# Optimization experiments

Hardware: AMD Instinct MI355X
Metric: run time of the kernel (lower is better)

## Reference

```python
import jax, jax.numpy as jnp
import numpy as np


def _mlp(x, w1, b1, w2, b2):
    # generic 2-layer MLP (stand-in for ConfiguredModule's combine_mlp / embedding_mlp)
    return jax.nn.gelu(x @ w1 + b1) @ w2 + b2


def setup_inputs() -> dict:
    key = jax.random.key(0)
    ks = jax.random.split(key, 8)
    B, N, A = 8, 128, 64          # molecules, atoms, nfeature
    Rr, Ra = 32, 16               # radial / angular geometry shifts
    P = N * (N - 1) // 2          # 8128 atom pairs
    d_pair, H, nembed = 32, 512, 256

    def rnd(k, shp, scale=1.0):
        return jax.random.normal(k, shp, dtype=jnp.float32) * scale

    return {
        "gr": rnd(ks[0], (B, N, Rr, N), 0.1),
        "ga": rnd(ks[1], (B, N, Ra, P), 0.1),
        "afv": rnd(ks[2], (B, N, A)),
        # combine_mlp: 2A -> 2A -> d_pair
        "cw1": rnd(ks[3], (2 * A, 2 * A), 1.0 / np.sqrt(2 * A)),
        "cb1": jnp.zeros((2 * A,), jnp.float32),
        "cw2": rnd(ks[4], (2 * A, d_pair), 1.0 / np.sqrt(2 * A)),
        "cb2": jnp.zeros((d_pair,), jnp.float32),
        # embedding_mlp: Rr*A + Ra*d_pair -> H -> nembed
        "ew1": rnd(ks[5], (Rr * A + Ra * d_pair, H), 1.0 / np.sqrt(Rr * A + Ra * d_pair)),
        "eb1": jnp.zeros((H,), jnp.float32),
        "ew2": rnd(ks[6], (H, nembed), 1.0 / np.sqrt(H)),
        "eb2": jnp.zeros((nembed,), jnp.float32),
    }


def reference(gr, ga, afv, cw1, cb1, cw2, cb2, ew1, eb1, ew2, eb2):
    B, N, A = afv.shape
    # _combine_afv_1: pairwise outer sum/product, upper-triangular (i<j) pairs.
    # Instead of materializing [B, 2A, N, N] and masking, gather pairs directly
    # (row-major i<j order matches torch's triu boolean-mask indexing).
    ii, jj = jnp.triu_indices(N, k=1)           # [P]
    ai = afv[:, ii, :]                           # [B, P, A]
    aj = afv[:, jj, :]                           # [B, P, A]
    afv_pair = jnp.concatenate([ai + aj, ai * aj], axis=-1)  # [B, P, 2A]
    afv_pair = _mlp(afv_pair, cw1, cb1, cw2, cb2)            # [B, P, d_pair]

    # grv = matmul(gr, afv[:, None]) : [B, N, Rr, N] @ [B, 1, N, A] -> [B, N, Rr, A]
    grv = jnp.einsum('bnrm,bma->bnra', gr, afv).reshape(B, N, -1)
    # gav = matmul(ga, afv_pair[:, None]) : [B, N, Ra, P] @ [B, 1, P, d] -> [B, N, Ra, d]
    gav = jnp.einsum('bnap,bpd->bnad', ga, afv_pair).reshape(B, N, -1)

    aef = _mlp(jnp.concatenate([grv, gav], axis=-1), ew1, eb1, ew2, eb2)  # [B, N, nembed]
    return aef, afv
```

## Files before the change

### kernel.cpp

```cpp
#include <hip/hip_runtime.h>
#include <math.h>

#define BB 8
#define NN 128
#define AA 64
#define RR 32
#define RA 16
#define PP 8128
#define DP 32
#define HH 512
#define EE 256
#define XDIM 2560

static constexpr size_t WS_PAIRT = 0;
static constexpr size_t WS_XB    = WS_PAIRT + (size_t)BB*DP*PP/2;
static constexpr size_t WS_EW1B  = WS_XB + (size_t)BB*NN*XDIM/2;
static constexpr size_t WS_CW1T  = WS_EW1B + (size_t)HH*XDIM/2;
static constexpr size_t WS_CW2T  = WS_CW1T + (size_t)128*128/2;
static constexpr size_t WS_EW2B  = WS_CW2T + (size_t)DP*128/2;
static constexpr size_t WS_HB    = WS_EW2B + (size_t)EE*HH/2;

typedef __attribute__((ext_vector_type(8))) short bf16x8;
typedef __attribute__((ext_vector_type(4))) float f32x4;

__device__ __forceinline__ float gelu_f(float x) {
    float u = 0.7978845608028654f * (x + 0.044715f * x * x * x);
    float au = fabsf(u);
    float e = __expf(-2.0f * au);
    float th = (1.0f - e) / (1.0f + e);
    th = copysignf(th, u);
    return 0.5f * x * (1.0f + th);
}

__device__ __forceinline__ unsigned short f2bf(float x) {
    union { float f; unsigned u; } v; v.f = x;
    unsigned r = v.u + 0x7fffu + ((v.u >> 16) & 1u);
    return (unsigned short)(r >> 16);
}

__device__ __forceinline__ bf16x8 pack_bf16x8(float4 a, float4 b) {
    bf16x8 r;
    r[0] = (short)f2bf(a.x); r[1] = (short)f2bf(a.y);
    r[2] = (short)f2bf(a.z); r[3] = (short)f2bf(a.w);
    r[4] = (short)f2bf(b.x); r[5] = (short)f2bf(b.y);
    r[6] = (short)f2bf(b.z); r[7] = (short)f2bf(b.w);
    return r;
}

__global__ __launch_bounds__(256) void prep_k(
    const float* __restrict__ cw1, const float* __restrict__ cw2,
    unsigned short* __restrict__ cw1T, unsigned short* __restrict__ cw2T)
{
    const int bid = blockIdx.x, t = threadIdx.x;
    if (bid < 16) {
        int idx = bid * 256 + t;
        int n = idx >> 5;
        int k0 = (idx & 31) * 4;
        ushort4 o;
        o.x = f2bf(cw1[(size_t)(k0 + 0) * 128 + n]);
        o.y = f2bf(cw1[(size_t)(k0 + 1) * 128 + n]);
        o.z = f2bf(cw1[(size_t)(k0 + 2) * 128 + n]);
        o.w = f2bf(cw1[(size_t)(k0 + 3) * 128 + n]);
        *(ushort4*)(cw1T + (size_t)n * 128 + k0) = o;
    } else {
        int idx = (bid - 16) * 256 + t;
        int d = idx >> 5;
        int k0 = (idx & 31) * 4;
        ushort4 o;
        o.x = f2bf(cw2[(size_t)(k0 + 0) * DP + d]);
        o.y = f2bf(cw2[(size_t)(k0 + 1) * DP + d]);
        o.z = f2bf(cw2[(size_t)(k0 + 2) * DP + d]);
        o.w = f2bf(cw2[(size_t)(k0 + 3) * DP + d]);
        *(ushort4*)(cw2T + (size_t)d * 128 + k0) = o;
    }
}

__global__ __launch_bounds__(256) void stage1_k(
    const float* __restrict__ afv, const unsigned short* __restrict__ cw1T,
    const float* __restrict__ cb1, const unsigned short* __restrict__ cw2T,
    const float* __restrict__ cb2, unsigned short* __restrict__ pairT)
{
    __shared__ unsigned short sm[16384];
    __shared__ int iis[64], jjs[64];
    const int bid = blockIdx.x;
    const int t = threadIdx.x;
    const int w = t >> 6, lane = t & 63;
    const int lm = lane & 15, lg = lane >> 4;

    const int b = bid / 127;
    const int pbase = (bid % 127) * 64;
    unsigned short* X = sm;
    unsigned short* Hs = sm + 8192;

    if (t < 64) {
        int p = pbase + t;
        int i = 0;
        while (i < 126) {
            int nx = i + 1;
            int off = nx * 127 - (nx * (nx - 1)) / 2;
            if (off <= p) i = nx; else break;
        }
        int off = i * 127 - (i * (i - 1)) / 2;
        iis[t] = i;
        jjs[t] = i + 1 + (p - off);
    }
    __syncthreads();
    {
        int pp = t & 63, seg = t >> 6;
        const float* ar = afv + (size_t)(b * NN + iis[pp]) * AA + seg * 16;
        const float* br = afv + (size_t)(b * NN + jjs[pp]) * AA + seg * 16;
        float4 xa = *(const float4*)(ar),     xb2 = *(const float4*)(ar + 4);
        float4 xc = *(const float4*)(ar + 8), xd = *(const float4*)(ar + 12);
        float4 ya = *(const float4*)(br),     yb = *(const float4*)(br + 4);
        float4 yc = *(const float4*)(br + 8), yd = *(const float4*)(br + 12);
        float4 s0 = make_float4(xa.x + ya.x, xa.y + ya.y, xa.z + ya.z, xa.w + ya.w);
        float4 s1 = make_float4(xb2.x + yb.x, xb2.y + yb.y, xb2.z + yb.z, xb2.w + yb.w);
        float4 s2 = make_float4(xc.x + yc.x, xc.y + yc.y, xc.z + yc.z, xc.w + yc.w);
        float4 s3 = make_float4(xd.x + yd.x, xd.y + yd.y, xd.z + yd.z, xd.w + yd.w);
        float4 p0 = make_float4(xa.x * ya.x, xa.y * ya.y, xa.z * ya.z, xa.w * ya.w);
        float4 p1 = make_float4(xb2.x * yb.x, xb2.y * yb.y, xb2.z * yb.z, xb2.w * yb.w);
        float4 p2 = make_float4(xc.x * yc.x, xc.y * yc.y, xc.z * yc.z, xc.w * yc.w);
        float4 p3 = make_float4(xd.x * yd.x, xd.y * yd.y, xd.z * yd.z, xd.w * yd.w);
        int gs = seg * 2, gp = 8 + seg * 2, sw = pp & 7;
        *(bf16x8*)(X + pp * 128 + (((gs + 0) ^ sw) * 8)) = pack_bf16x8(s0, s1);
        *(bf16x8*)(X + pp * 128 + (((gs + 1) ^ sw) * 8)) = pack_bf16x8(s2, s3);
        *(bf16x8*)(X + pp * 128 + (((gp + 0) ^ sw) * 8)) = pack_bf16x8(p0, p1);
        *(bf16x8*)(X + pp * 128 + (((gp + 1) ^ sw) * 8)) = pack_bf16x8(p2, p3);
    }
    __syncthreads();
    const int wn = w * 32;
    f32x4 acc1[4][2];
    #pragma unroll
    for (int i = 0; i < 4; ++i)
        #pragma unroll
        for (int j = 0; j < 2; ++j) acc1[i][j] = 0.f;
    #pragma unroll
    for (int ks = 0; ks < 4; ++ks) {
        int g = ks * 4 + lg;
        bf16x8 a[4];
        #pragma unroll
        for (int mi = 0; mi < 4; ++mi) {
            int row = mi * 16 + lm;
            a[mi] = *(const bf16x8*)(X + row * 128 + ((g ^ (row & 7)) * 8));
        }
        #pragma unroll
        for (int ni = 0; ni < 2; ++ni) {
            bf16x8 bv = *(const bf16x8*)(cw1T + (size_t)(wn + ni * 16 + lm) * 128 +
                                         ks * 32 + lg * 8);
            #pragma unroll
            for (int mi = 0; mi < 4; ++mi)
                acc1[mi][ni] = __builtin_amdgcn_mfma_f32_16x16x32_bf16(
                    a[mi], bv, acc1[mi][ni], 0, 0, 0);
        }
    }
    #pragma unroll
    for (int ni = 0; ni < 2; ++ni) {
        int n = wn + ni * 16 + lm;
        float bb = cb1[n];
        int gn = n >> 3, ne = n & 7;
        #pragma unroll
        for (int mi = 0; mi < 4; ++mi)
            #pragma unroll
            for (int r = 0; r < 4; ++r) {
                int row = mi * 16 + lg * 4 + r;
                Hs[row * 128 + ((gn ^ (row & 7)) * 8 + ne)] =
                    f2bf(gelu_f(acc1[mi][ni][r] + bb));
            }
    }
    __syncthreads();
    f32x4 acc2[2];
    acc2[0] = 0.f; acc2[1] = 0.f;
    #pragma unroll
    for (int ks = 0; ks < 4; ++ks) {
        int row = w * 16 + lm;
        int g = ks * 4 + lg;
        bf16x8 a2 = *(const bf16x8*)(Hs + row * 128 + ((g ^ (row & 7)) * 8));
        #pragma unroll
        for (int ni = 0; ni < 2; ++ni) {
            bf16x8 bv = *(const bf16x8*)(cw2T + (size_t)(ni * 16 + lm) * 128 +
                                         ks * 32 + lg * 8);
            acc2[ni] = __builtin_amdgcn_mfma_f32_16x16x32_bf16(a2, bv, acc2[ni], 0, 0, 0);
        }
    }
    {
        unsigned short* T = sm;
        __syncthreads();
        #pragma unroll
        for (int ni = 0; ni < 2; ++ni) {
            int d = ni * 16 + lm;
            float bb = cb2[d];
            #pragma unroll
            for (int r = 0; r < 4; ++r) {
                int p = w * 16 + lg * 4 + r;
                T[d * 64 + p] = f2bf(acc2[ni][r] + bb);
            }
        }
        __syncthreads();
        int d = t >> 3, slot = t & 7;
        bf16x8 v = *(const bf16x8*)(T + d * 64 + slot * 8);
        *(bf16x8*)(pairT + ((size_t)b * DP + d) * PP + pbase + slot * 8) = v;
    }
}

__global__ __launch_bounds__(256) void gav_k(
    const float* __restrict__ ga, const unsigned short* __restrict__ pairT,
    unsigned short* __restrict__ Xb,
    const float* __restrict__ gr, const float* __restrict__ afv,
    const float* __restrict__ ew1, unsigned short* __restrict__ ew1bT,
    const float* __restrict__ ew2, unsigned short* __restrict__ ew2bT,
    float* __restrict__ out2)
{
    __shared__ unsigned short sm[24576];
    const int bid = blockIdx.x;
    const int t = threadIdx.x;
    const int w = t >> 6, lane = t & 63;
    const int lm = lane & 15, lg = lane >> 4;

    if (bid >= 2176) {
        int idx = (bid - 2176) * 256 + t;
        float4 v = *(const float4*)(afv + (size_t)idx * 4);
        *(float4*)(out2 + (size_t)idx * 4) = v;
        return;
    }
    if (bid >= 2048) {
        int q = (bid - 2048) * 256 + t;
        int n = q & 255;
        int k0 = (q >> 8) * 4;
        ushort4 o;
        o.x = f2bf(ew2[(size_t)(k0 + 0) * EE + n]);
        o.y = f2bf(ew2[(size_t)(k0 + 1) * EE + n]);
        o.z = f2bf(ew2[(size_t)(k0 + 2) * EE + n]);
        o.w = f2bf(ew2[(size_t)(k0 + 3) * EE + n]);
        *(ushort4*)(ew2bT + (size_t)n * HH + k0) = o;
        return;
    }
    if (bid >= 768) {
        int q = (bid - 768) * 256 + t;
        int n = q & 511;
        int k0 = (q >> 9) * 4;
        ushort4 o;
        o.x = f2bf(ew1[(size_t)(k0 + 0) * HH + n]);
        o.y = f2bf(ew1[(size_t)(k0 + 1) * HH + n]);
        o.z = f2bf(ew1[(size_t)(k0 + 2) * HH + n]);
        o.w = f2bf(ew1[(size_t)(k0 + 3) * HH + n]);
        *(ushort4*)(ew1bT + (size_t)n * XDIM + k0) = o;
        return;
    }

    if (bid >= 512) {
        const int gb = bid - 512;
        const int b = gb >> 5;
        const int rbase = (gb & 31) * 128;
        const float* gab = gr + ((size_t)b * 4096 + rbase) * NN;
        unsigned short* As  = sm;
        unsigned short* Bs2 = sm + 16384;
        {
            const int srow = t >> 1, half = t & 1;
            const float* arow = gab + (size_t)srow * NN + half * 64;
            #pragma unroll
            for (int q = 0; q < 8; ++q) {
                float4 x0 = *(const float4*)(arow + q * 8);
                float4 x1 = *(const float4*)(arow + q * 8 + 4);
                bf16x8 v = pack_bf16x8(x0, x1);
                int g = half * 8 + q;
                *(bf16x8*)(As + srow * 128 + ((g ^ (srow & 7)) * 8)) = v;
            }
        }
        #pragma unroll
        for (int q = 0; q < 8; ++q) {
            int pos = t + q * 256;
            int m = pos >> 4, f4i = pos & 15;
            float4 v = *(const float4*)(afv + (size_t)(b * NN + m) * AA + f4i * 4);
            int gm = m >> 3, me = m & 7;
            float vv[4] = {v.x, v.y, v.z, v.w};
            #pragma unroll
            for (int i = 0; i < 4; ++i) {
                int a = f4i * 4 + i;
                Bs2[a * 128 + ((gm ^ (a & 7)) * 8 + me)] = f2bf(vv[i]);
            }
        }
        __syncthreads();
        const int wm = w * 32;
        f32x4 acc[2][4];
        #pragma unroll
        for (int i = 0; i < 2; ++i)
            #pragma unroll
            for (int j = 0; j < 4; ++j) acc[i][j] = 0.f;
        #pragma unroll
        for (int ks = 0; ks < 4; ++ks) {
            int g = ks * 4 + lg;
            int r0 = wm + lm, r1 = wm + 16 + lm;
            bf16x8 a0 = *(const bf16x8*)(As + r0 * 128 + ((g ^ (r0 & 7)) * 8));
            bf16x8 a1 = *(const bf16x8*)(As + r1 * 128 + ((g ^ (r1 & 7)) * 8));
            #pragma unroll
            for (int ni = 0; ni < 4; ++ni) {
                int a = ni * 16 + lm;
                bf16x8 bv = *(const bf16x8*)(Bs2 + a * 128 + ((g ^ (a & 7)) * 8));
                acc[0][ni] = __builtin_amdgcn_mfma_f32_16x16x32_bf16(a0, bv, acc[0][ni], 0, 0, 0);
                acc[1][ni] = __builtin_amdgcn_mfma_f32_16x16x32_bf16(a1, bv, acc[1][ni], 0, 0, 0);
            }
        }
        __syncthreads();
        unsigned short* T = sm;
        #pragma unroll
        for (int mi = 0; mi < 2; ++mi)
            #pragma unroll
            for (int ni = 0; ni < 4; ++ni)
                #pragma unroll
                for (int r = 0; r < 4; ++r)
                    T[(wm + mi * 16 + lg * 4 + r) * 64 + ni * 16 + lm] =
                        f2bf(acc[mi][ni][r]);
        __syncthreads();
        #pragma unroll
        for (int q = 0; q < 4; ++q) {
            int idx = t + q * 256;
            int rr2 = idx >> 3, slot = idx & 7;
            bf16x8 v = *(const bf16x8*)(T + rr2 * 64 + slot * 8);
            int grow = rbase + rr2;
            *(bf16x8*)(Xb + ((size_t)(b * NN) + (grow >> 5)) * XDIM +
                       (grow & 31) * 64 + slot * 8) = v;
        }
        return;
    }

    const int b = bid & 7, rt = bid >> 3;
    const int rbase = rt * 32;
    const int srow = t >> 3, slot = t & 7;
    const int wr = (w & 1) * 16, wc = (w >> 1) * 16;

    f32x4 acc = 0.f;

    const float* gab = ga + (size_t)(b * 2048 + rbase) * PP;
    const unsigned short* pbT = pairT + (size_t)b * DP * PP;

    float4 ra[4];
    bf16x8 rb0, rb1;

#define GAV_LOAD(IT)                                                         \
    {                                                                        \
        int kn = (IT) * 128 + slot * 8;                                      \
        int k1 = kn + 64; if (k1 > PP - 8) k1 = PP - 8;                      \
        ra[0] = *(const float4*)(gab + (size_t)srow * PP + kn);              \
        ra[1] = *(const float4*)(gab + (size_t)srow * PP + kn + 4);          \
        ra[2] = *(const float4*)(gab + (size_t)srow * PP + k1);              \
        ra[3] = *(const float4*)(gab + (size_t)srow * PP + k1 + 4);          \
        rb0 = *(const bf16x8*)(pbT + (size_t)srow * PP + kn);                \
        rb1 = *(const bf16x8*)(pbT + (size_t)srow * PP + k1);                \
    }

#define GAV_WRITE(BUF)                                                      \
    {                                                                        \
        unsigned short* A_ = sm + (BUF) * 8192;                              \
        unsigned short* B_ = A_ + 4096;                                      \
        const int sw_ = srow & 7;                                            \
        const int g0_ = (slot ^ sw_) * 8;                                    \
        const int g1_ = ((slot ^ sw_) + 8) * 8;                              \
        *(bf16x8*)(A_ + srow * 128 + g0_) = pack_bf16x8(ra[0], ra[1]);       \
        *(bf16x8*)(A_ + srow * 128 + g1_) = pack_bf16x8(ra[2], ra[3]);       \
        *(bf16x8*)(B_ + srow * 128 + g0_) = rb0;                             \
        *(bf16x8*)(B_ + srow * 128 + g1_) = rb1;                             \
    }

    GAV_LOAD(0);
    GAV_WRITE(0);
    __syncthreads();
    GAV_LOAD(1);

    for (int it = 0; it < 64; ++it) {
        const int cur = it & 1;
        const unsigned short* Ac = sm + cur * 8192;
        const unsigned short* Bc = Ac + 4096;
        if (it + 1 < 64) GAV_WRITE(cur ^ 1);
        if (it + 2 < 64) GAV_LOAD(it + 2);
        if (it < 63) {
            #pragma unroll
            for (int ks = 0; ks < 4; ++ks) {
                int gg = ks * 4 + lg;
                int rowa = wr + lm;
                int rowb = wc + lm;
                bf16x8 a  = *(const bf16x8*)(Ac + rowa * 128 + ((gg ^ (rowa & 7)) * 8));
                bf16x8 bv = *(const bf16x8*)(Bc + rowb * 128 + ((gg ^ (rowb & 7)) * 8));
                acc = __builtin_amdgcn_mfma_f32_16x16x32_bf16(a, bv, acc, 0, 0, 0);
            }
        } else {
            #pragma unroll
            for (int ks = 0; ks < 2; ++ks) {
                int gg = ks * 4 + lg;
                int rowa = wr + lm;
                int rowb = wc + lm;
                bf16x8 a  = *(const bf16x8*)(Ac + rowa * 128 + ((gg ^ (rowa & 7)) * 8));
                bf16x8 bv = *(const bf16x8*)(Bc + rowb * 128 + ((gg ^ (rowb & 7)) * 8));
                acc = __builtin_amdgcn_mfma_f32_16x16x32_bf16(a, bv, acc, 0, 0, 0);
            }
        }
        __syncthreads();
    }
    #pragma unroll
    for (int r = 0; r < 4; ++r) {
        int grow = rbase + wr + lg * 4 + r;
        int n = grow >> 4, a2 = grow & 15;
        int d = wc + lm;
        Xb[(size_t)(b * NN + n) * XDIM + 2048 + a2 * DP + d] = f2bf(acc[r]);
    }
}

__global__ __launch_bounds__(256) void mlp1_k(
    const unsigned short* __restrict__ Xb,
    const unsigned short* __restrict__ Wt,
    const float* __restrict__ eb1, unsigned short* __restrict__ Hb)
{
    __shared__ unsigned short sm[8192];
    const int bid = blockIdx.x;
    const int xcd = bid & 7, idx = bid >> 3;
    const int rt = (xcd << 2) | (idx & 3);
    const int ct = idx >> 2;
    const int rbase = rt * 32, nbase = ct * 32;
    const int t = threadIdx.x;
    const int w = t >> 6, lane = t & 63;
    const int lm = lane & 15, lg = lane >> 4;
    const int wr = (w & 1) * 16, wc = (w >> 1) * 16;
    const int srow = t >> 3, sg = t & 7;

    f32x4 acc = 0.f;

    const unsigned short* Arow = Xb + (size_t)(rbase + srow) * XDIM;
    const unsigned short* Brow = Wt + (size_t)(nbase + srow) * XDIM;

    bf16x8 rA, rB;

#define M1_LOAD(IT)  { rA = *(const bf16x8*)(Arow + (IT) * 64 + sg * 8);     \
                       rB = *(const bf16x8*)(Brow + (IT) * 64 + sg * 8); }
#define M1_WRITE(BUF) { unsigned short* A_ = sm + (BUF) * 4096;              \
                        unsigned short* B_ = A_ + 2048;                      \
                        const int sw_ = srow & 7;                            \
                        *(bf16x8*)(A_ + srow * 64 + ((sg ^ sw_) * 8)) = rA;  \
                        *(bf16x8*)(B_ + srow * 64 + ((sg ^ sw_) * 8)) = rB; }

    M1_LOAD(0); M1_WRITE(0);
    __syncthreads();
    M1_LOAD(1);

    for (int it = 0; it < 40; ++it) {
        const int cur = it & 1;
        const unsigned short* Ac = sm + cur * 4096;
        const unsigned short* Bc = Ac + 2048;
        if (it + 1 < 40) M1_WRITE(cur ^ 1);
        if (it + 2 < 40) M1_LOAD(it + 2);
        #pragma unroll
        for (int ks = 0; ks < 2; ++ks) {
            int g = ks * 4 + lg;
            int r0 = wr + lm, r1 = wc + lm;
            bf16x8 a  = *(const bf16x8*)(Ac + r0 * 64 + ((g ^ (r0 & 7)) * 8));
            bf16x8 bv = *(const bf16x8*)(Bc + r1 * 64 + ((g ^ (r1 & 7)) * 8));
            acc = __builtin_amdgcn_mfma_f32_16x16x32_bf16(a, bv, acc, 0, 0, 0);
        }
        __syncthreads();
    }
    const int col = nbase + wc + lm;
    const float bb = eb1[col];
    #pragma unroll
    for (int r = 0; r < 4; ++r) {
        int row = rbase + wr + lg * 4 + r;
        Hb[(size_t)row * HH + col] = f2bf(gelu_f(acc[r] + bb));
    }
}

__global__ __launch_bounds__(256) void mlp2_k(
    const unsigned short* __restrict__ Hb,
    const unsigned short* __restrict__ Wt,
    const float* __restrict__ eb2, float* __restrict__ out)
{
    __shared__ unsigned short sm[8192];
    const int bid = blockIdx.x;
    const int xcd = bid & 7, idx = bid >> 3;
    const int rt = (xcd << 2) | (idx & 3);
    const int ct = idx >> 2;
    const int rbase = rt * 32, nbase = ct * 32;
    const int t = threadIdx.x;
    const int w = t >> 6, lane = t & 63;
    const int lm = lane & 15, lg = lane >> 4;
    const int wr = (w & 1) * 16, wc = (w >> 1) * 16;
    const int srow = t >> 3, sg = t & 7;

    f32x4 acc = 0.f;

    const unsigned short* Arow = Hb + (size_t)(rbase + srow) * HH;
    const unsigned short* Brow = Wt + (size_t)(nbase + srow) * HH;

    bf16x8 rA, rB;

#define M2_LOAD(IT)  { rA = *(const bf16x8*)(Arow + (IT) * 64 + sg * 8);     \
                       rB = *(const bf16x8*)(Brow + (IT) * 64 + sg * 8); }
#define M2_WRITE(BUF) { unsigned short* A_ = sm + (BUF) * 4096;              \
                        unsigned short* B_ = A_ + 2048;                      \
                        const int sw_ = srow & 7;                            \
                        *(bf16x8*)(A_ + srow * 64 + ((sg ^ sw_) * 8)) = rA;  \
                        *(bf16x8*)(B_ + srow * 64 + ((sg ^ sw_) * 8)) = rB; }

    M2_LOAD(0); M2_WRITE(0);
    __syncthreads();
    M2_LOAD(1);

    for (int it = 0; it < 8; ++it) {
        const int cur = it & 1;
        const unsigned short* Ac = sm + cur * 4096;
        const unsigned short* Bc = Ac + 2048;
        if (it + 1 < 8) M2_WRITE(cur ^ 1);
        if (it + 2 < 8) M2_LOAD(it + 2);
        #pragma unroll
        for (int ks = 0; ks < 2; ++ks) {
            int g = ks * 4 + lg;
            int r0 = wr + lm, r1 = wc + lm;
            bf16x8 a  = *(const bf16x8*)(Ac + r0 * 64 + ((g ^ (r0 & 7)) * 8));
            bf16x8 bv = *(const bf16x8*)(Bc + r1 * 64 + ((g ^ (r1 & 7)) * 8));
            acc = __builtin_amdgcn_mfma_f32_16x16x32_bf16(a, bv, acc, 0, 0, 0);
        }
        __syncthreads();
    }
    const int col = nbase + wc + lm;
    const float bb = eb2[col];
    #pragma unroll
    for (int r = 0; r < 4; ++r) {
        int row = rbase + wr + lg * 4 + r;
        out[(size_t)row * EE + col] = acc[r] + bb;
    }
}

extern "C" void kernel_launch(void* const* d_in, const int* in_sizes, int n_in,
                              void* d_out, int out_size, void* d_ws, size_t ws_size,
                              hipStream_t stream) {
    const float* gr  = (const float*)d_in[0];
    const float* ga  = (const float*)d_in[1];
    const float* afv = (const float*)d_in[2];
    const float* cw1 = (const float*)d_in[3];
    const float* cb1 = (const float*)d_in[4];
    const float* cw2 = (const float*)d_in[5];
    const float* cb2 = (const float*)d_in[6];
    const float* ew1 = (const float*)d_in[7];
    const float* eb1 = (const float*)d_in[8];
    const float* ew2 = (const float*)d_in[9];
    const float* eb2 = (const float*)d_in[10];
    float* out = (float*)d_out;
    float* ws = (float*)d_ws;

    unsigned short* pairT  = (unsigned short*)(ws + WS_PAIRT);
    unsigned short* Xb     = (unsigned short*)(ws + WS_XB);
    unsigned short* ew1bT  = (unsigned short*)(ws + WS_EW1B);
    unsigned short* cw1T   = (unsigned short*)(ws + WS_CW1T);
    unsigned short* cw2T   = (unsigned short*)(ws + WS_CW2T);
    unsigned short* ew2bT  = (unsigned short*)(ws + WS_EW2B);
    unsigned short* Hb     = (unsigned short*)(ws + WS_HB);

    prep_k<<<dim3(20), dim3(256), 0, stream>>>(cw1, cw2, cw1T, cw2T);
    stage1_k<<<dim3(1016), dim3(256), 0, stream>>>(afv, cw1T, cb1, cw2T, cb2, pairT);
    gav_k<<<dim3(2240), dim3(256), 0, stream>>>(ga, pairT, Xb, gr, afv,
                                                ew1, ew1bT, ew2, ew2bT,
                                                out + (size_t)BB * NN * EE);
    mlp1_k<<<dim3(512), dim3(256), 0, stream>>>(Xb, ew1bT, eb1, Hb);
    mlp2_k<<<dim3(256), dim3(256), 0, stream>>>(Hb, ew2bT, eb2, out);
}
```

Measured before the change: 171.0 us.

## Shrink gav/grv tiles for more blocks and deepen K-step in MLP GEMMs

The ga-projection blocks now each cover 16 ga rows, which is one atom, instead of 32. This doubles the block count to 1024 and lowers LDS use to spread the bandwidth-bound ga stream over more workgroups. Only two of the four waves issue MFMAs, so compute per block goes partly idle. The grv path is likewise split into 64-row tiles. The mlp1/mlp2 GEMMs load 128-wide K slices per stage instead of 64, halving the loop iterations and barriers at the cost of more LDS.

```diff
diff --git a/kernel.cpp b/kernel.cpp
--- a/kernel.cpp
+++ b/kernel.cpp
@@ -210,20 +210,20 @@
     const float* __restrict__ ew2, unsigned short* __restrict__ ew2bT,
     float* __restrict__ out2)
 {
-    __shared__ unsigned short sm[24576];
+    __shared__ unsigned short sm[16384];
     const int bid = blockIdx.x;
     const int t = threadIdx.x;
     const int w = t >> 6, lane = t & 63;
     const int lm = lane & 15, lg = lane >> 4;
 
-    if (bid >= 2176) {
-        int idx = (bid - 2176) * 256 + t;
+    if (bid >= 2944) {
+        int idx = (bid - 2944) * 256 + t;
         float4 v = *(const float4*)(afv + (size_t)idx * 4);
         *(float4*)(out2 + (size_t)idx * 4) = v;
         return;
     }
-    if (bid >= 2048) {
-        int q = (bid - 2048) * 256 + t;
+    if (bid >= 2816) {
+        int q = (bid - 2816) * 256 + t;
         int n = q & 255;
         int k0 = (q >> 8) * 4;
         ushort4 o;
@@ -234,8 +234,8 @@
         *(ushort4*)(ew2bT + (size_t)n * HH + k0) = o;
         return;
     }
-    if (bid >= 768) {
-        int q = (bid - 768) * 256 + t;
+    if (bid >= 1536) {
+        int q = (bid - 1536) * 256 + t;
         int n = q & 511;
         int k0 = (q >> 9) * 4;
         ushort4 o;
@@ -247,23 +247,23 @@
         return;
     }
 
-    if (bid >= 512) {
-        const int gb = bid - 512;
-        const int b = gb >> 5;
-        const int rbase = (gb & 31) * 128;
+    if (bid >= 1024) {
+        const int gb = bid - 1024;
+        const int b = gb >> 6;
+        const int rbase = (gb & 63) * 64;
         const float* gab = gr + ((size_t)b * 4096 + rbase) * NN;
         unsigned short* As  = sm;
-        unsigned short* Bs2 = sm + 16384;
+        unsigned short* Bs2 = sm + 8192;
         {
-            const int srow = t >> 1, half = t & 1;
-            const float* arow = gab + (size_t)srow * NN + half * 64;
-            #pragma unroll
-            for (int q = 0; q < 8; ++q) {
-                float4 x0 = *(const float4*)(arow + q * 8);
-                float4 x1 = *(const float4*)(arow + q * 8 + 4);
+            const int srow2 = t >> 2, q4 = t & 3;
+            const float* arow = gab + (size_t)srow2 * NN + q4 * 32;
+            #pragma unroll
+            for (int j = 0; j < 4; ++j) {
+                float4 x0 = *(const float4*)(arow + j * 8);
+                float4 x1 = *(const float4*)(arow + j * 8 + 4);
                 bf16x8 v = pack_bf16x8(x0, x1);
-                int g = half * 8 + q;
-                *(bf16x8*)(As + srow * 128 + ((g ^ (srow & 7)) * 8)) = v;
+                int g = 4 * q4 + j;
+                *(bf16x8*)(As + srow2 * 128 + ((g ^ (srow2 & 7)) * 8)) = v;
             }
         }
         #pragma unroll
@@ -280,39 +280,32 @@
             }
         }
         __syncthreads();
-        const int wm = w * 32;
-        f32x4 acc[2][4];
-        #pragma unroll
-        for (int i = 0; i < 2; ++i)
-            #pragma unroll
-            for (int j = 0; j < 4; ++j) acc[i][j] = 0.f;
+        const int wm = w * 16;
+        f32x4 acc[4];
+        #pragma unroll
+        for (int j = 0; j < 4; ++j) acc[j] = 0.f;
         #pragma unroll
         for (int ks = 0; ks < 4; ++ks) {
             int g = ks * 4 + lg;
-            int r0 = wm + lm, r1 = wm + 16 + lm;
+            int r0 = wm + lm;
             bf16x8 a0 = *(const bf16x8*)(As + r0 * 128 + ((g ^ (r0 & 7)) * 8));
-            bf16x8 a1 = *(const bf16x8*)(As + r1 * 128 + ((g ^ (r1 & 7)) * 8));
             #pragma unroll
             for (int ni = 0; ni < 4; ++ni) {
                 int a = ni * 16 + lm;
                 bf16x8 bv = *(const bf16x8*)(Bs2 + a * 128 + ((g ^ (a & 7)) * 8));
-                acc[0][ni] = __builtin_amdgcn_mfma_f32_16x16x32_bf16(a0, bv, acc[0][ni], 0, 0, 0);
-                acc[1][ni] = __builtin_amdgcn_mfma_f32_16x16x32_bf16(a1, bv, acc[1][ni], 0, 0, 0);
+                acc[ni] = __builtin_amdgcn_mfma_f32_16x16x32_bf16(a0, bv, acc[ni], 0, 0, 0);
             }
         }
         __syncthreads();
         unsigned short* T = sm;
         #pragma unroll
-        for (int mi = 0; mi < 2; ++mi)
-            #pragma unroll
-            for (int ni = 0; ni < 4; ++ni)
-                #pragma unroll
-                for (int r = 0; r < 4; ++r)
-                    T[(wm + mi * 16 + lg * 4 + r) * 64 + ni * 16 + lm] =
-                        f2bf(acc[mi][ni][r]);
-        __syncthreads();
-        #pragma unroll
-        for (int q = 0; q < 4; ++q) {
+        for (int ni = 0; ni < 4; ++ni)
+            #pragma unroll
+            for (int r = 0; r < 4; ++r)
+                T[(wm + lg * 4 + r) * 64 + ni * 16 + lm] = f2bf(acc[ni][r]);
+        __syncthreads();
+        #pragma unroll
+        for (int q = 0; q < 2; ++q) {
             int idx = t + q * 256;
             int rr2 = idx >> 3, slot = idx & 7;
             bf16x8 v = *(const bf16x8*)(T + rr2 * 64 + slot * 8);
@@ -324,41 +317,40 @@
     }
 
     const int b = bid & 7, rt = bid >> 3;
-    const int rbase = rt * 32;
-    const int srow = t >> 3, slot = t & 7;
-    const int wr = (w & 1) * 16, wc = (w >> 1) * 16;
+    const int rbase = rt * 16;
+    const int srow = t >> 4, slot = t & 15;
+    const int bd = t >> 3, bslot = t & 7;
+    const int wc = w * 16;
 
     f32x4 acc = 0.f;
 
     const float* gab = ga + (size_t)(b * 2048 + rbase) * PP;
     const unsigned short* pbT = pairT + (size_t)b * DP * PP;
 
-    float4 ra[4];
+    float4 ra0, ra1;
     bf16x8 rb0, rb1;
 
 #define GAV_LOAD(IT)                                                         \
     {                                                                        \
         int kn = (IT) * 128 + slot * 8;                                      \
-        int k1 = kn + 64; if (k1 > PP - 8) k1 = PP - 8;                      \
-        ra[0] = *(const float4*)(gab + (size_t)srow * PP + kn);              \
-        ra[1] = *(const float4*)(gab + (size_t)srow * PP + kn + 4);          \
-        ra[2] = *(const float4*)(gab + (size_t)srow * PP + k1);              \
-        ra[3] = *(const float4*)(gab + (size_t)srow * PP + k1 + 4);          \
-        rb0 = *(const bf16x8*)(pbT + (size_t)srow * PP + kn);                \
-        rb1 = *(const bf16x8*)(pbT + (size_t)srow * PP + k1);                \
+        if (kn > PP - 8) kn = PP - 8;           \
+        ra0 = *(const float4*)(gab + (size_t)srow * PP + kn);                \
+        ra1 = *(const float4*)(gab + (size_t)srow * PP + kn + 4);            \
+        int kb = (IT) * 128 + bslot * 8;                                     \
+        int kb1 = kb + 64; if (kb1 > PP - 8) kb1 = PP - 8;                   \
+        rb0 = *(const bf16x8*)(pbT + (size_t)bd * PP + kb);                  \
+        rb1 = *(const bf16x8*)(pbT + (size_t)bd * PP + kb1);                 \
     }
 
 #define GAV_WRITE(BUF)                                                      \
     {                                                                        \
-        unsigned short* A_ = sm + (BUF) * 8192;                              \
-        unsigned short* B_ = A_ + 4096;                                      \
-        const int sw_ = srow & 7;                                            \
-        const int g0_ = (slot ^ sw_) * 8;                                    \
-        const int g1_ = ((slot ^ sw_) + 8) * 8;                              \
-        *(bf16x8*)(A_ + srow * 128 + g0_) = pack_bf16x8(ra[0], ra[1]);       \
-        *(bf16x8*)(A_ + srow * 128 + g1_) = pack_bf16x8(ra[2], ra[3]);       \
-        *(bf16x8*)(B_ + srow * 128 + g0_) = rb0;                             \
-        *(bf16x8*)(B_ + srow * 128 + g1_) = rb1;                             \
+        unsigned short* A_ = sm + (BUF) * 6144;                              \
+        unsigned short* B_ = A_ + 2048;                                      \
+        int gA = slot ^ (srow & 7);                                          \
+        *(bf16x8*)(A_ + srow * 128 + gA * 8) = pack_bf16x8(ra0, ra1);        \
+        int gB = bslot ^ (bd & 7);                                           \
+        *(bf16x8*)(B_ + bd * 128 + gB * 8) = rb0;                            \
+        *(bf16x8*)(B_ + bd * 128 + (gB + 8) * 8) = rb1;                      \
     }
 
     GAV_LOAD(0);
@@ -368,39 +360,28 @@
 
     for (int it = 0; it < 64; ++it) {
         const int cur = it & 1;
-        const unsigned short* Ac = sm + cur * 8192;
-        const unsigned short* Bc = Ac + 4096;
+        const unsigned short* Ac = sm + cur * 6144;
+        const unsigned short* Bc = Ac + 2048;
         if (it + 1 < 64) GAV_WRITE(cur ^ 1);
         if (it + 2 < 64) GAV_LOAD(it + 2);
-        if (it < 63) {
-            #pragma unroll
-            for (int ks = 0; ks < 4; ++ks) {
+        if (w < 2) {
+            const int nk = (it < 63) ? 4 : 2;
+            for (int ks = 0; ks < nk; ++ks) {
                 int gg = ks * 4 + lg;
-                int rowa = wr + lm;
                 int rowb = wc + lm;
-                bf16x8 a  = *(const bf16x8*)(Ac + rowa * 128 + ((gg ^ (rowa & 7)) * 8));
+                bf16x8 a  = *(const bf16x8*)(Ac + lm * 128 + ((gg ^ (lm & 7)) * 8));
                 bf16x8 bv = *(const bf16x8*)(Bc + rowb * 128 + ((gg ^ (rowb & 7)) * 8));
                 acc = __builtin_amdgcn_mfma_f32_16x16x32_bf16(a, bv, acc, 0, 0, 0);
             }
-        } else {
-            #pragma unroll
-            for (int ks = 0; ks < 2; ++ks) {
-                int gg = ks * 4 + lg;
-                int rowa = wr + lm;
-                int rowb = wc + lm;
-                bf16x8 a  = *(const bf16x8*)(Ac + rowa * 128 + ((gg ^ (rowa & 7)) * 8));
-                bf16x8 bv = *(const bf16x8*)(Bc + rowb * 128 + ((gg ^ (rowb & 7)) * 8));
-                acc = __builtin_amdgcn_mfma_f32_16x16x32_bf16(a, bv, acc, 0, 0, 0);
-            }
-        }
-        __syncthreads();
-    }
-    #pragma unroll
-    for (int r = 0; r < 4; ++r) {
-        int grow = rbase + wr + lg * 4 + r;
-        int n = grow >> 4, a2 = grow & 15;
-        int d = wc + lm;
-        Xb[(size_t)(b * NN + n) * XDIM + 2048 + a2 * DP + d] = f2bf(acc[r]);
+        }
+        __syncthreads();
+    }
+    if (w < 2) {
+        #pragma unroll
+        for (int r = 0; r < 4; ++r) {
+            int a2 = lg * 4 + r;
+            Xb[(size_t)(b * NN + rt) * XDIM + 2048 + a2 * DP + wc + lm] = f2bf(acc[r]);
+        }
     }
 }
 
@@ -409,7 +390,7 @@
     const unsigned short* __restrict__ Wt,
     const float* __restrict__ eb1, unsigned short* __restrict__ Hb)
 {
-    __shared__ unsigned short sm[8192];
+    __shared__ unsigned short sm[16384];
     const int bid = blockIdx.x;
     const int xcd = bid & 7, idx = bid >> 3;
     const int rt = (xcd << 2) | (idx & 3);
@@ -426,32 +407,37 @@
     const unsigned short* Arow = Xb + (size_t)(rbase + srow) * XDIM;
     const unsigned short* Brow = Wt + (size_t)(nbase + srow) * XDIM;
 
-    bf16x8 rA, rB;
-
-#define M1_LOAD(IT)  { rA = *(const bf16x8*)(Arow + (IT) * 64 + sg * 8);     \
-                       rB = *(const bf16x8*)(Brow + (IT) * 64 + sg * 8); }
-#define M1_WRITE(BUF) { unsigned short* A_ = sm + (BUF) * 4096;              \
-                        unsigned short* B_ = A_ + 2048;                      \
-                        const int sw_ = srow & 7;                            \
-                        *(bf16x8*)(A_ + srow * 64 + ((sg ^ sw_) * 8)) = rA;  \
-                        *(bf16x8*)(B_ + srow * 64 + ((sg ^ sw_) * 8)) = rB; }
+    bf16x8 rA0, rA1, rB0, rB1;
+
+#define M1_LOAD(IT)  { int kn = (IT) * 128 + sg * 8;                         \
+                       rA0 = *(const bf16x8*)(Arow + kn);                    \
+                       rA1 = *(const bf16x8*)(Arow + kn + 64);               \
+                       rB0 = *(const bf16x8*)(Brow + kn);                    \
+                       rB1 = *(const bf16x8*)(Brow + kn + 64); }
+#define M1_WRITE(BUF) { unsigned short* A_ = sm + (BUF) * 8192;              \
+                        unsigned short* B_ = A_ + 4096;                      \
+                        int g0 = sg ^ (srow & 7);                            \
+                        *(bf16x8*)(A_ + srow * 128 + g0 * 8) = rA0;          \
+                        *(bf16x8*)(A_ + srow * 128 + (g0 + 8) * 8) = rA1;    \
+                        *(bf16x8*)(B_ + srow * 128 + g0 * 8) = rB0;          \
+                        *(bf16x8*)(B_ + srow * 128 + (g0 + 8) * 8) = rB1; }
 
     M1_LOAD(0); M1_WRITE(0);
     __syncthreads();
     M1_LOAD(1);
 
-    for (int it = 0; it < 40; ++it) {
+    for (int it = 0; it < 20; ++it) {
         const int cur = it & 1;
-        const unsigned short* Ac = sm + cur * 4096;
-        const unsigned short* Bc = Ac + 2048;
-        if (it + 1 < 40) M1_WRITE(cur ^ 1);
-        if (it + 2 < 40) M1_LOAD(it + 2);
-        #pragma unroll
-        for (int ks = 0; ks < 2; ++ks) {
+        const unsigned short* Ac = sm + cur * 8192;
+        const unsigned short* Bc = Ac + 4096;
+        if (it + 1 < 20) M1_WRITE(cur ^ 1);
+        if (it + 2 < 20) M1_LOAD(it + 2);
+        #pragma unroll
+        for (int ks = 0; ks < 4; ++ks) {
             int g = ks * 4 + lg;
             int r0 = wr + lm, r1 = wc + lm;
-            bf16x8 a  = *(const bf16x8*)(Ac + r0 * 64 + ((g ^ (r0 & 7)) * 8));
-            bf16x8 bv = *(const bf16x8*)(Bc + r1 * 64 + ((g ^ (r1 & 7)) * 8));
+            bf16x8 a  = *(const bf16x8*)(Ac + r0 * 128 + ((g ^ (r0 & 7)) * 8));
+            bf16x8 bv = *(const bf16x8*)(Bc + r1 * 128 + ((g ^ (r1 & 7)) * 8));
             acc = __builtin_amdgcn_mfma_f32_16x16x32_bf16(a, bv, acc, 0, 0, 0);
         }
         __syncthreads();
@@ -470,7 +456,7 @@
     const unsigned short* __restrict__ Wt,
     const float* __restrict__ eb2, float* __restrict__ out)
 {
-    __shared__ unsigned short sm[8192];
+    __shared__ unsigned short sm[16384];
     const int bid = blockIdx.x;
     const int xcd = bid & 7, idx = bid >> 3;
     const int rt = (xcd << 2) | (idx & 3);
@@ -487,32 +473,37 @@
     const unsigned short* Arow = Hb + (size_t)(rbase + srow) * HH;
     const unsigned short* Brow = Wt + (size_t)(nbase + srow) * HH;
 
-    bf16x8 rA, rB;
-
-#define M2_LOAD(IT)  { rA = *(const bf16x8*)(Arow + (IT) * 64 + sg * 8);     \
-                       rB = *(const bf16x8*)(Brow + (IT) * 64 + sg * 8); }
-#define M2_WRITE(BUF) { unsigned short* A_ = sm + (BUF) * 4096;              \
-                        unsigned short* B_ = A_ + 2048;                      \
-                        const int sw_ = srow & 7;                            \
-                        *(bf16x8*)(A_ + srow * 64 + ((sg ^ sw_) * 8)) = rA;  \
-                        *(bf16x8*)(B_ + srow * 64 + ((sg ^ sw_) * 8)) = rB; }
+    bf16x8 rA0, rA1, rB0, rB1;
+
+#define M2_LOAD(IT)  { int kn = (IT) * 128 + sg * 8;                         \
+                       rA0 = *(const bf16x8*)(Arow + kn);                    \
+                       rA1 = *(const bf16x8*)(Arow + kn + 64);               \
+                       rB0 = *(const bf16x8*)(Brow + kn);                    \
+                       rB1 = *(const bf16x8*)(Brow + kn + 64); }
+#define M2_WRITE(BUF) { unsigned short* A_ = sm + (BUF) * 8192;              \
+                        unsigned short* B_ = A_ + 4096;                      \
+                        int g0 = sg ^ (srow & 7);                            \
+                        *(bf16x8*)(A_ + srow * 128 + g0 * 8) = rA0;          \
+                        *(bf16x8*)(A_ + srow * 128 + (g0 + 8) * 8) = rA1;    \
+                        *(bf16x8*)(B_ + srow * 128 + g0 * 8) = rB0;          \
+                        *(bf16x8*)(B_ + srow * 128 + (g0 + 8) * 8) = rB1; }
 
     M2_LOAD(0); M2_WRITE(0);
     __syncthreads();
     M2_LOAD(1);
 
-    for (int it = 0; it < 8; ++it) {
+    for (int it = 0; it < 4; ++it) {
         const int cur = it & 1;
-        const unsigned short* Ac = sm + cur * 4096;
-        const unsigned short* Bc = Ac + 2048;
-        if (it + 1 < 8) M2_WRITE(cur ^ 1);
-        if (it + 2 < 8) M2_LOAD(it + 2);
-        #pragma unroll
-        for (int ks = 0; ks < 2; ++ks) {
+        const unsigned short* Ac = sm + cur * 8192;
+        const unsigned short* Bc = Ac + 4096;
+        if (it + 1 < 4) M2_WRITE(cur ^ 1);
+        if (it + 2 < 4) M2_LOAD(it + 2);
+        #pragma unroll
+        for (int ks = 0; ks < 4; ++ks) {
             int g = ks * 4 + lg;
             int r0 = wr + lm, r1 = wc + lm;
-            bf16x8 a  = *(const bf16x8*)(Ac + r0 * 64 + ((g ^ (r0 & 7)) * 8));
-            bf16x8 bv = *(const bf16x8*)(Bc + r1 * 64 + ((g ^ (r1 & 7)) * 8));
+            bf16x8 a  = *(const bf16x8*)(Ac + r0 * 128 + ((g ^ (r0 & 7)) * 8));
+            bf16x8 bv = *(const bf16x8*)(Bc + r1 * 128 + ((g ^ (r1 & 7)) * 8));
             acc = __builtin_amdgcn_mfma_f32_16x16x32_bf16(a, bv, acc, 0, 0, 0);
         }
         __syncthreads();
@@ -553,7 +544,7 @@
 
     prep_k<<<dim3(20), dim3(256), 0, stream>>>(cw1, cw2, cw1T, cw2T);
     stage1_k<<<dim3(1016), dim3(256), 0, stream>>>(afv, cw1T, cb1, cw2T, cb2, pairT);
-    gav_k<<<dim3(2240), dim3(256), 0, stream>>>(ga, pairT, Xb, gr, afv,
+    gav_k<<<dim3(3008), dim3(256), 0, stream>>>(ga, pairT, Xb, gr, afv,
                                                 ew1, ew1bT, ew2, ew2bT,
                                                 out + (size_t)BB * NN * EE);
     mlp1_k<<<dim3(512), dim3(256), 0, stream>>>(Xb, ew1bT, eb1, Hb);
```

New measurement: 162.3 us (median of 2 runs). 5.1% less time.
